# Kernel optimization log

Measured on AMD Instinct MI355X. Metric: run time of the kernel, lower is better.

Reference implementation:

```python
import jax, jax.numpy as jnp
import numpy as np

B = 262144      # batch
DIN = 100       # input covariate dim (cfg_density[0][0])
H = 64          # hidden dim
G = 10          # num_grid -> density output dim G+1
NH = 5          # number of dosage-bucket heads in Multi_head


def setup_inputs() -> dict:
    key = jax.random.key(0)
    ks = jax.random.split(key, 16)
    s = 0.05
    return {
        "dosage": jax.random.uniform(ks[0], (B,), dtype=jnp.float32),
        "x": jax.random.normal(ks[1], (B, DIN), dtype=jnp.float32),
        # density feature MLP (two Linear+ReLU layers)
        "dW0": jax.random.normal(ks[2], (DIN, H), dtype=jnp.float32) * s,
        "db0": jax.random.normal(ks[3], (H,), dtype=jnp.float32) * s,
        "dW1": jax.random.normal(ks[4], (H, H), dtype=jnp.float32) * s,
        "db1": jax.random.normal(ks[5], (H,), dtype=jnp.float32) * s,
        # Density_Block: Linear(H -> G+1) then softmax + grid interpolation
        "dbW": jax.random.normal(ks[6], (H, G + 1), dtype=jnp.float32) * s,
        "dbB": jax.random.normal(ks[7], (G + 1,), dtype=jnp.float32) * s,
        # Multi_head: 5 structurally identical heads, params stacked on axis 0
        # layer0: Treat_Linear(64 -> 64, relu, istreat=1)
        "W0": jax.random.normal(ks[8], (NH, H, H), dtype=jnp.float32) * s,
        "tw0": jax.random.normal(ks[9], (NH, H), dtype=jnp.float32) * s,
        "b0": jax.random.normal(ks[10], (NH, H), dtype=jnp.float32) * s,
        # layer1 (last): Treat_Linear(64 -> 1, no act, istreat=1)
        "W1": jax.random.normal(ks[11], (NH, H, 1), dtype=jnp.float32) * s,
        "tw1": jax.random.normal(ks[12], (NH, 1), dtype=jnp.float32) * s,
        "b1": jax.random.normal(ks[13], (NH, 1), dtype=jnp.float32) * s,
    }


def reference(dosage, x, dW0, db0, dW1, db1, dbW, dbB, W0, tw0, b0, W1, tw1, b1):
    # hidden feature MLP
    hidden = jax.nn.relu(x @ dW0 + db0)
    hidden = jax.nn.relu(hidden @ dW1 + db1)            # [B, H]

    # ---- Density_Block: softmax over grid, dual gather + linear interpolation
    p = jax.nn.softmax(hidden @ dbW + dbB, axis=1)      # [B, G+1]
    tB = dosage * G
    U = jnp.ceil(tB)
    inter = 1.0 - (U - tB)                              # fractional position in cell
    Ui = U.astype(jnp.int32)
    Li = Ui - 1
    Li = Li + (Li < 0).astype(jnp.int32)                # clamp L=-1 -> 0
    pL = jnp.take_along_axis(p, Li[:, None], axis=1)[:, 0]
    pU = jnp.take_along_axis(p, Ui[:, None], axis=1)[:, 0]
    g = pL + (pU - pL) * inter                          # [B]

    # ---- Multi_head: 5 heads on dosage buckets [0,.2),[.2,.4),...,[.8,1.)
    t = dosage
    # layer0: out = feat @ W + t * tw + b, relu; compute all heads, select later
    h0 = jax.nn.relu(
        jnp.einsum('bi,hio->bho', hidden, W0)
        + t[:, None, None] * tw0[None]
        + b0[None]
    )                                                   # [B, NH, H]
    # last layer: no activation
    out1 = (jnp.einsum('bho,hoj->bhj', h0, W1)
            + t[:, None, None] * tw1[None]
            + b1[None])                                 # [B, NH, 1]
    bucket = jnp.clip(jnp.floor(t * NH).astype(jnp.int32), 0, NH - 1)
    Q = jnp.take_along_axis(out1, bucket[:, None, None], axis=1)[:, 0, :]  # [B, 1]
    return g, Q
```

## Files before the change

kernel.cpp:

```cpp
#include <hip/hip_runtime.h>

typedef __attribute__((ext_vector_type(8))) short  short8;
typedef __attribute__((ext_vector_type(4))) float  floatx4;
typedef __attribute__((ext_vector_type(4))) int    intx4;

constexpr int DIN = 100;
constexpr int H   = 64;
constexpr int G   = 10;
constexpr int NH  = 5;
constexpr int MWG = 64;
constexpr int HP  = 72;

constexpr int NF_DW0 = 16, NF_DW1 = 8, NF_DBW = 2;
constexpr int NF_LIN = NF_DW0 + NF_DW1 + NF_DBW;
constexpr int NF_TOT = NF_LIN + 40;

__device__ __forceinline__ unsigned short f2bf_rne(float f) {
    union { float f; unsigned u; } v{f};
    unsigned r = v.u + 0x7FFF + ((v.u >> 16) & 1);
    return (unsigned short)(r >> 16);
}

__device__ __forceinline__ short8 pack8(const float* f) {
    intx4 p;
    #pragma unroll
    for (int j = 0; j < 4; ++j) {
        unsigned a = __float_as_uint(f[2 * j])     + 0x8000u;
        unsigned b = __float_as_uint(f[2 * j + 1]) + 0x8000u;
        p[j] = (int)((b & 0xFFFF0000u) | (a >> 16));
    }
    union { intx4 i; short8 s; } u; u.i = p;
    return u.s;
}

__device__ __forceinline__ unsigned short f2bf_hu(float f) {
    return (unsigned short)((__float_as_uint(f) + 0x8000u) >> 16);
}

__device__ __forceinline__ short8 ldfrag(const unsigned short* __restrict__ ws,
                                         int f, int lane) {
    return *(const short8*)(ws + (size_t)(f * 64 + lane) * 8);
}

__global__ __launch_bounds__(64) void pack_kernel(
    const float* __restrict__ dW0, const float* __restrict__ dW1,
    const float* __restrict__ dbW, const float* __restrict__ W0,
    unsigned short* __restrict__ ws)
{
    const int f = blockIdx.x;
    const int lane = threadIdx.x;
    const int q = lane >> 4, cl = lane & 15;
    float v[8];
    if (f < NF_DW0) {
        int c = f >> 2, g = f & 3;
        #pragma unroll
        for (int j = 0; j < 8; ++j) {
            int k = c * 32 + q * 8 + j, n = g * 16 + cl;
            v[j] = (k < DIN) ? dW0[k * H + n] : 0.0f;
        }
    } else if (f < NF_DW0 + NF_DW1) {
        int r = f - NF_DW0; int c = r >> 2, g = r & 3;
        #pragma unroll
        for (int j = 0; j < 8; ++j) {
            int k = c * 32 + q * 8 + j, n = g * 16 + cl;
            v[j] = dW1[k * H + n];
        }
    } else if (f < NF_LIN) {
        int c = f - (NF_DW0 + NF_DW1);
        #pragma unroll
        for (int j = 0; j < 8; ++j) {
            int k = c * 32 + q * 8 + j, n = cl;
            v[j] = (n <= G) ? dbW[k * (G + 1) + n] : 0.0f;
        }
    } else {
        int r = f - NF_LIN; int h = r >> 3; r &= 7; int c = r >> 2, g = r & 3;
        #pragma unroll
        for (int j = 0; j < 8; ++j) {
            int k = c * 32 + q * 8 + j, n = g * 16 + cl;
            v[j] = W0[(h * H + k) * H + n];
        }
    }
    short8 s;
    #pragma unroll
    for (int j = 0; j < 8; ++j) s[j] = (short)f2bf_rne(v[j]);
    *(short8*)(ws + (size_t)(f * 64 + lane) * 8) = s;
}

__global__ __launch_bounds__(256, 4) void drnet_mfma(
    const float* __restrict__ dosage, const float* __restrict__ x,
    const float* __restrict__ db0, const float* __restrict__ db1,
    const float* __restrict__ dbB,
    const float* __restrict__ tw0, const float* __restrict__ b0,
    const float* __restrict__ W1, const float* __restrict__ tw1,
    const float* __restrict__ b1,
    const unsigned short* __restrict__ wsfrag,
    float* __restrict__ outg, float* __restrict__ outq)
{
    __shared__ unsigned short hbuf[MWG * HP];
    const int tid  = threadIdx.x;
    const int wave = tid >> 6, lane = tid & 63;
    const int q = lane >> 4, cl = lane & 15;
    const int rowbase = blockIdx.x * MWG + wave * 16;
    unsigned short* hb = hbuf + wave * 16 * HP;

    float t4[4];
    int   bk4[4];
    #pragma unroll
    for (int r = 0; r < 4; ++r) {
        float t = dosage[rowbase + 4 * q + r];
        t4[r] = t;
        int bk = (int)floorf(t * (float)NH);
        bk4[r] = min(max(bk, 0), NH - 1);
    }

    floatx4 acc[4];

    short8 a1[4];
    {
        const float* xr = x + (size_t)(rowbase + cl) * DIN;
        #pragma unroll
        for (int cch = 0; cch < 4; ++cch) {
            float f[8];
            if (cch < 3) {
                floatx4 u0 = *(const floatx4*)(xr + cch * 32 + q * 8);
                floatx4 u1 = *(const floatx4*)(xr + cch * 32 + q * 8 + 4);
                f[0]=u0.x; f[1]=u0.y; f[2]=u0.z; f[3]=u0.w;
                f[4]=u1.x; f[5]=u1.y; f[6]=u1.z; f[7]=u1.w;
            } else {
                if (q == 0) {
                    floatx4 u0 = *(const floatx4*)(xr + 96);
                    f[0]=u0.x; f[1]=u0.y; f[2]=u0.z; f[3]=u0.w;
                    f[4]=f[5]=f[6]=f[7]=0.0f;
                } else {
                    #pragma unroll
                    for (int j = 0; j < 8; ++j) f[j] = 0.0f;
                }
            }
            a1[cch] = pack8(f);
        }
    }
    #pragma unroll
    for (int g = 0; g < 4; ++g) acc[g] = (floatx4)0.0f;
    #pragma unroll
    for (int cch = 0; cch < 4; ++cch)
        #pragma unroll
        for (int g = 0; g < 4; ++g) {
            short8 bf = ldfrag(wsfrag, cch * 4 + g, lane);
            acc[g] = __builtin_amdgcn_mfma_f32_16x16x32_bf16(a1[cch], bf, acc[g], 0, 0, 0);
        }
    #pragma unroll
    for (int g = 0; g < 4; ++g) {
        float bias = db0[g * 16 + cl];
        #pragma unroll
        for (int r = 0; r < 4; ++r)
            hb[(4 * q + r) * HP + g * 16 + cl] =
                f2bf_hu(fmaxf(acc[g][r] + bias, 0.0f));
    }

    short8 a2[2];
    #pragma unroll
    for (int cch = 0; cch < 2; ++cch)
        a2[cch] = *(const short8*)(hb + cl * HP + cch * 32 + q * 8);
    #pragma unroll
    for (int g = 0; g < 4; ++g) acc[g] = (floatx4)0.0f;
    #pragma unroll
    for (int cch = 0; cch < 2; ++cch)
        #pragma unroll
        for (int g = 0; g < 4; ++g) {
            short8 bf = ldfrag(wsfrag, NF_DW0 + cch * 4 + g, lane);
            acc[g] = __builtin_amdgcn_mfma_f32_16x16x32_bf16(a2[cch], bf, acc[g], 0, 0, 0);
        }
    #pragma unroll
    for (int g = 0; g < 4; ++g) {
        float bias = db1[g * 16 + cl];
        #pragma unroll
        for (int r = 0; r < 4; ++r)
            hb[(4 * q + r) * HP + g * 16 + cl] =
                f2bf_hu(fmaxf(acc[g][r] + bias, 0.0f));
    }

    short8 af[2];
    #pragma unroll
    for (int cch = 0; cch < 2; ++cch)
        af[cch] = *(const short8*)(hb + cl * HP + cch * 32 + q * 8);

    floatx4 accd = (floatx4)0.0f;
    #pragma unroll
    for (int cch = 0; cch < 2; ++cch) {
        short8 bf = ldfrag(wsfrag, NF_DW0 + NF_DW1 + cch, lane);
        accd = __builtin_amdgcn_mfma_f32_16x16x32_bf16(af[cch], bf, accd, 0, 0, 0);
    }
    const float dbBv = (cl <= G) ? dbB[cl] : 0.0f;
    float gout[4];
    #pragma unroll
    for (int r = 0; r < 4; ++r) {
        float l = (cl <= G) ? (accd[r] + dbBv) : -1e30f;
        float m = l;
        m = fmaxf(m, __shfl_xor(m, 1)); m = fmaxf(m, __shfl_xor(m, 2));
        m = fmaxf(m, __shfl_xor(m, 4)); m = fmaxf(m, __shfl_xor(m, 8));
        float e = __expf(l - m);
        float s = e;
        s += __shfl_xor(s, 1); s += __shfl_xor(s, 2);
        s += __shfl_xor(s, 4); s += __shfl_xor(s, 8);
        const float t  = t4[r];
        const float tB = t * (float)G;
        const float U  = ceilf(tB);
        const float inter = 1.0f - (U - tB);
        int Ui = (int)U; int Li = Ui - 1; if (Li < 0) Li = 0;
        float pL = __shfl(e, q * 16 + Li);
        float pU = __shfl(e, q * 16 + Ui);
        gout[r] = (pL + (pU - pL) * inter) / s;
    }
    if (cl == 0) {
        floatx4 gv = { gout[0], gout[1], gout[2], gout[3] };
        *(floatx4*)(outg + rowbase + 4 * q) = gv;
    }

    float asel[4][4];
    #pragma unroll
    for (int g = 0; g < 4; ++g)
        #pragma unroll
        for (int r = 0; r < 4; ++r) asel[g][r] = 0.0f;

    #pragma unroll 1
    for (int h = 0; h < NH; ++h) {
        floatx4 acch[4];
        #pragma unroll
        for (int g = 0; g < 4; ++g) acch[g] = (floatx4)0.0f;
        #pragma unroll
        for (int cch = 0; cch < 2; ++cch)
            #pragma unroll
            for (int g = 0; g < 4; ++g) {
                short8 bf = ldfrag(wsfrag, NF_LIN + h * 8 + cch * 4 + g, lane);
                acch[g] = __builtin_amdgcn_mfma_f32_16x16x32_bf16(af[cch], bf, acch[g], 0, 0, 0);
            }
        #pragma unroll
        for (int r = 0; r < 4; ++r) {
            bool sel = (bk4[r] == h);
            #pragma unroll
            for (int g = 0; g < 4; ++g)
                asel[g][r] = sel ? acch[g][r] : asel[g][r];
        }
    }

    float qp[4] = {0, 0, 0, 0};
    #pragma unroll
    for (int g = 0; g < 4; ++g) {
        const int ci = g * 16 + cl;
        #pragma unroll
        for (int r = 0; r < 4; ++r) {
            const int off = bk4[r] * H + ci;
            float h0 = asel[g][r] + t4[r] * tw0[off] + b0[off];
            qp[r] += fmaxf(h0, 0.0f) * W1[off];
        }
    }
    #pragma unroll
    for (int r = 0; r < 4; ++r) {
        float s = qp[r];
        s += __shfl_xor(s, 1); s += __shfl_xor(s, 2);
        s += __shfl_xor(s, 4); s += __shfl_xor(s, 8);
        const int h = bk4[r];
        qp[r] = s + t4[r] * tw1[h] + b1[h];
    }
    if (cl == 0) {
        floatx4 Qv = { qp[0], qp[1], qp[2], qp[3] };
        *(floatx4*)(outq + rowbase + 4 * q) = Qv;
    }
}

extern "C" void kernel_launch(void* const* d_in, const int* in_sizes, int n_in,
                              void* d_out, int out_size, void* d_ws, size_t ws_size,
                              hipStream_t stream) {
    const float* dosage = (const float*)d_in[0];
    const float* x      = (const float*)d_in[1];
    const float* dW0    = (const float*)d_in[2];
    const float* db0    = (const float*)d_in[3];
    const float* dW1    = (const float*)d_in[4];
    const float* db1    = (const float*)d_in[5];
    const float* dbW    = (const float*)d_in[6];
    const float* dbB    = (const float*)d_in[7];
    const float* W0     = (const float*)d_in[8];
    const float* tw0    = (const float*)d_in[9];
    const float* b0     = (const float*)d_in[10];
    const float* W1     = (const float*)d_in[11];
    const float* tw1    = (const float*)d_in[12];
    const float* b1     = (const float*)d_in[13];

    const int Btot = in_sizes[0];
    float* outg = (float*)d_out;
    float* outq = outg + Btot;
    unsigned short* ws = (unsigned short*)d_ws;

    pack_kernel<<<NF_TOT, 64, 0, stream>>>(dW0, dW1, dbW, W0, ws);
    drnet_mfma<<<Btot / MWG, 256, 0, stream>>>(dosage, x, db0, db1, dbB,
                                               tw0, b0, W1, tw1, b1,
                                               ws, outg, outq);
}
```

Before: 210.4 us.

## Compute transposed MFMA layers in registers, dropping LDS staging and raising rows per wave

Swaps the MFMA operands so weights are the A operand and activations the B operand, which gives each lane an output layout where a row sits in lanes. The hidden activations are then re-laid between layers with cross-lane shuffles instead of being staged through shared memory. Each wave now handles 32 rows as two 16-row tiles, and head weights are loaded once per head and reused across both tiles. The softmax and head bias/ReLU/W1 stage use vectorized parameter loads, and the softmax no longer subtracts the row max. In exchange there are more shuffles and higher register pressure, and dropping the max subtraction could overflow the exponential for large logits.

```diff
diff --git a/kernel.cpp b/kernel.cpp
--- a/kernel.cpp
+++ b/kernel.cpp
@@ -1,15 +1,14 @@
 #include <hip/hip_runtime.h>
+#include <hip/hip_bf16.h>
 
 typedef __attribute__((ext_vector_type(8))) short  short8;
 typedef __attribute__((ext_vector_type(4))) float  floatx4;
-typedef __attribute__((ext_vector_type(4))) int    intx4;
 
 constexpr int DIN = 100;
 constexpr int H   = 64;
 constexpr int G   = 10;
 constexpr int NH  = 5;
-constexpr int MWG = 64;
-constexpr int HP  = 72;
+constexpr int MWG = 128;
 
 constexpr int NF_DW0 = 16, NF_DW1 = 8, NF_DBW = 2;
 constexpr int NF_LIN = NF_DW0 + NF_DW1 + NF_DBW;
@@ -21,21 +20,13 @@
     return (unsigned short)(r >> 16);
 }
 
-__device__ __forceinline__ short8 pack8(const float* f) {
-    intx4 p;
-    #pragma unroll
-    for (int j = 0; j < 4; ++j) {
-        unsigned a = __float_as_uint(f[2 * j])     + 0x8000u;
-        unsigned b = __float_as_uint(f[2 * j + 1]) + 0x8000u;
-        p[j] = (int)((b & 0xFFFF0000u) | (a >> 16));
-    }
-    union { intx4 i; short8 s; } u; u.i = p;
-    return u.s;
-}
-
-__device__ __forceinline__ unsigned short f2bf_hu(float f) {
-    return (unsigned short)((__float_as_uint(f) + 0x8000u) >> 16);
-}
+__device__ __forceinline__ unsigned pkbf(float a, float b) {
+    union { __hip_bfloat162 h; unsigned u; } u;
+    u.h = __float22bfloat162_rn(make_float2(a, b));
+    return u.u;
+}
+
+union frag_u { unsigned u[4]; short8 s; };
 
 __device__ __forceinline__ short8 ldfrag(const unsigned short* __restrict__ ws,
                                          int f, int lane) {
@@ -86,7 +77,25 @@
     *(short8*)(ws + (size_t)(f * 64 + lane) * 8) = s;
 }
 
-__global__ __launch_bounds__(256, 4) void drnet_mfma(
+__device__ __forceinline__ void transp(const unsigned P[4][2], int q, int cl,
+                                       unsigned out[2][4]) {
+    const int sL = (((2 * q) & 3) << 4) | cl;
+    const int sH = (((2 * q + 1) & 3) << 4) | cl;
+    const bool hi = (q >= 2);
+    #pragma unroll
+    for (int c2 = 0; c2 < 2; ++c2)
+        #pragma unroll
+        for (int w = 0; w < 2; ++w) {
+            int a0 = __shfl((int)P[2 * c2][w], sL);
+            int a1 = __shfl((int)P[2 * c2 + 1][w], sL);
+            out[c2][w] = (unsigned)(hi ? a1 : a0);
+            int b0 = __shfl((int)P[2 * c2][w], sH);
+            int b1 = __shfl((int)P[2 * c2 + 1][w], sH);
+            out[c2][2 + w] = (unsigned)(hi ? b1 : b0);
+        }
+}
+
+__global__ __launch_bounds__(256, 4) void drnet_t(
     const float* __restrict__ dosage, const float* __restrict__ x,
     const float* __restrict__ db0, const float* __restrict__ db1,
     const float* __restrict__ dbB,
@@ -96,175 +105,162 @@
     const unsigned short* __restrict__ wsfrag,
     float* __restrict__ outg, float* __restrict__ outq)
 {
-    __shared__ unsigned short hbuf[MWG * HP];
     const int tid  = threadIdx.x;
     const int wave = tid >> 6, lane = tid & 63;
     const int q = lane >> 4, cl = lane & 15;
-    const int rowbase = blockIdx.x * MWG + wave * 16;
-    unsigned short* hb = hbuf + wave * 16 * HP;
-
-    float t4[4];
-    int   bk4[4];
-    #pragma unroll
-    for (int r = 0; r < 4; ++r) {
-        float t = dosage[rowbase + 4 * q + r];
-        t4[r] = t;
-        int bk = (int)floorf(t * (float)NH);
-        bk4[r] = min(max(bk, 0), NH - 1);
-    }
-
-    floatx4 acc[4];
-
-    short8 a1[4];
-    {
-        const float* xr = x + (size_t)(rowbase + cl) * DIN;
-        #pragma unroll
-        for (int cch = 0; cch < 4; ++cch) {
+    const int rowbase = blockIdx.x * MWG + wave * 32;
+
+    float tmt[2]; int bkmt[2];
+    #pragma unroll
+    for (int mt = 0; mt < 2; ++mt) {
+        float t = dosage[rowbase + mt * 16 + cl];
+        tmt[mt] = t;
+        bkmt[mt] = min(max((int)floorf(t * (float)NH), 0), NH - 1);
+    }
+
+    unsigned af[2][2][4];
+
+    #pragma unroll 1
+    for (int mt = 0; mt < 2; ++mt) {
+        unsigned xf[4][4];
+        const float* xr = x + (size_t)(rowbase + mt * 16 + cl) * DIN;
+        #pragma unroll
+        for (int c = 0; c < 4; ++c) {
             float f[8];
-            if (cch < 3) {
-                floatx4 u0 = *(const floatx4*)(xr + cch * 32 + q * 8);
-                floatx4 u1 = *(const floatx4*)(xr + cch * 32 + q * 8 + 4);
+            if (c < 3) {
+                floatx4 u0 = *(const floatx4*)(xr + c * 32 + q * 8);
+                floatx4 u1 = *(const floatx4*)(xr + c * 32 + q * 8 + 4);
                 f[0]=u0.x; f[1]=u0.y; f[2]=u0.z; f[3]=u0.w;
                 f[4]=u1.x; f[5]=u1.y; f[6]=u1.z; f[7]=u1.w;
+            } else if (q == 0) {
+                floatx4 u0 = *(const floatx4*)(xr + 96);
+                f[0]=u0.x; f[1]=u0.y; f[2]=u0.z; f[3]=u0.w;
+                f[4]=f[5]=f[6]=f[7]=0.0f;
             } else {
-                if (q == 0) {
-                    floatx4 u0 = *(const floatx4*)(xr + 96);
-                    f[0]=u0.x; f[1]=u0.y; f[2]=u0.z; f[3]=u0.w;
-                    f[4]=f[5]=f[6]=f[7]=0.0f;
-                } else {
-                    #pragma unroll
-                    for (int j = 0; j < 8; ++j) f[j] = 0.0f;
-                }
+                #pragma unroll
+                for (int j = 0; j < 8; ++j) f[j] = 0.0f;
             }
-            a1[cch] = pack8(f);
-        }
-    }
-    #pragma unroll
-    for (int g = 0; g < 4; ++g) acc[g] = (floatx4)0.0f;
-    #pragma unroll
-    for (int cch = 0; cch < 4; ++cch)
-        #pragma unroll
-        for (int g = 0; g < 4; ++g) {
-            short8 bf = ldfrag(wsfrag, cch * 4 + g, lane);
-            acc[g] = __builtin_amdgcn_mfma_f32_16x16x32_bf16(a1[cch], bf, acc[g], 0, 0, 0);
-        }
-    #pragma unroll
-    for (int g = 0; g < 4; ++g) {
-        float bias = db0[g * 16 + cl];
-        #pragma unroll
-        for (int r = 0; r < 4; ++r)
-            hb[(4 * q + r) * HP + g * 16 + cl] =
-                f2bf_hu(fmaxf(acc[g][r] + bias, 0.0f));
-    }
-
-    short8 a2[2];
-    #pragma unroll
-    for (int cch = 0; cch < 2; ++cch)
-        a2[cch] = *(const short8*)(hb + cl * HP + cch * 32 + q * 8);
-    #pragma unroll
-    for (int g = 0; g < 4; ++g) acc[g] = (floatx4)0.0f;
-    #pragma unroll
-    for (int cch = 0; cch < 2; ++cch)
-        #pragma unroll
-        for (int g = 0; g < 4; ++g) {
-            short8 bf = ldfrag(wsfrag, NF_DW0 + cch * 4 + g, lane);
-            acc[g] = __builtin_amdgcn_mfma_f32_16x16x32_bf16(a2[cch], bf, acc[g], 0, 0, 0);
-        }
-    #pragma unroll
-    for (int g = 0; g < 4; ++g) {
-        float bias = db1[g * 16 + cl];
-        #pragma unroll
-        for (int r = 0; r < 4; ++r)
-            hb[(4 * q + r) * HP + g * 16 + cl] =
-                f2bf_hu(fmaxf(acc[g][r] + bias, 0.0f));
-    }
-
-    short8 af[2];
-    #pragma unroll
-    for (int cch = 0; cch < 2; ++cch)
-        af[cch] = *(const short8*)(hb + cl * HP + cch * 32 + q * 8);
-
-    floatx4 accd = (floatx4)0.0f;
-    #pragma unroll
-    for (int cch = 0; cch < 2; ++cch) {
-        short8 bf = ldfrag(wsfrag, NF_DW0 + NF_DW1 + cch, lane);
-        accd = __builtin_amdgcn_mfma_f32_16x16x32_bf16(af[cch], bf, accd, 0, 0, 0);
-    }
-    const float dbBv = (cl <= G) ? dbB[cl] : 0.0f;
-    float gout[4];
-    #pragma unroll
-    for (int r = 0; r < 4; ++r) {
-        float l = (cl <= G) ? (accd[r] + dbBv) : -1e30f;
-        float m = l;
-        m = fmaxf(m, __shfl_xor(m, 1)); m = fmaxf(m, __shfl_xor(m, 2));
-        m = fmaxf(m, __shfl_xor(m, 4)); m = fmaxf(m, __shfl_xor(m, 8));
-        float e = __expf(l - m);
-        float s = e;
-        s += __shfl_xor(s, 1); s += __shfl_xor(s, 2);
-        s += __shfl_xor(s, 4); s += __shfl_xor(s, 8);
-        const float t  = t4[r];
+            xf[c][0] = pkbf(f[0], f[1]); xf[c][1] = pkbf(f[2], f[3]);
+            xf[c][2] = pkbf(f[4], f[5]); xf[c][3] = pkbf(f[6], f[7]);
+        }
+        floatx4 acc[4];
+        #pragma unroll
+        for (int f = 0; f < 4; ++f) acc[f] = (floatx4)0.0f;
+        #pragma unroll
+        for (int c = 0; c < 4; ++c) {
+            frag_u b; b.u[0]=xf[c][0]; b.u[1]=xf[c][1]; b.u[2]=xf[c][2]; b.u[3]=xf[c][3];
+            #pragma unroll
+            for (int f = 0; f < 4; ++f)
+                acc[f] = __builtin_amdgcn_mfma_f32_16x16x32_bf16(
+                    ldfrag(wsfrag, c * 4 + f, lane), b.s, acc[f], 0, 0, 0);
+        }
+        unsigned P[4][2];
+        #pragma unroll
+        for (int f = 0; f < 4; ++f) {
+            floatx4 b4 = *(const floatx4*)(db0 + f * 16 + 4 * q);
+            float v0 = fmaxf(acc[f][0] + b4[0], 0.0f);
+            float v1 = fmaxf(acc[f][1] + b4[1], 0.0f);
+            float v2 = fmaxf(acc[f][2] + b4[2], 0.0f);
+            float v3 = fmaxf(acc[f][3] + b4[3], 0.0f);
+            P[f][0] = pkbf(v0, v1); P[f][1] = pkbf(v2, v3);
+        }
+        unsigned hf[2][4];
+        transp(P, q, cl, hf);
+
+        #pragma unroll
+        for (int f = 0; f < 4; ++f) acc[f] = (floatx4)0.0f;
+        #pragma unroll
+        for (int c2 = 0; c2 < 2; ++c2) {
+            frag_u b; b.u[0]=hf[c2][0]; b.u[1]=hf[c2][1]; b.u[2]=hf[c2][2]; b.u[3]=hf[c2][3];
+            #pragma unroll
+            for (int f = 0; f < 4; ++f)
+                acc[f] = __builtin_amdgcn_mfma_f32_16x16x32_bf16(
+                    ldfrag(wsfrag, NF_DW0 + c2 * 4 + f, lane), b.s, acc[f], 0, 0, 0);
+        }
+        #pragma unroll
+        for (int f = 0; f < 4; ++f) {
+            floatx4 b4 = *(const floatx4*)(db1 + f * 16 + 4 * q);
+            float v0 = fmaxf(acc[f][0] + b4[0], 0.0f);
+            float v1 = fmaxf(acc[f][1] + b4[1], 0.0f);
+            float v2 = fmaxf(acc[f][2] + b4[2], 0.0f);
+            float v3 = fmaxf(acc[f][3] + b4[3], 0.0f);
+            P[f][0] = pkbf(v0, v1); P[f][1] = pkbf(v2, v3);
+        }
+        transp(P, q, cl, af[mt]);
+
+        floatx4 accd = (floatx4)0.0f;
+        #pragma unroll
+        for (int c2 = 0; c2 < 2; ++c2) {
+            frag_u b; b.u[0]=af[mt][c2][0]; b.u[1]=af[mt][c2][1];
+            b.u[2]=af[mt][c2][2]; b.u[3]=af[mt][c2][3];
+            accd = __builtin_amdgcn_mfma_f32_16x16x32_bf16(
+                ldfrag(wsfrag, NF_DW0 + NF_DW1 + c2, lane), b.s, accd, 0, 0, 0);
+        }
+        float e[4];
+        #pragma unroll
+        for (int r = 0; r < 4; ++r) {
+            int gi = 4 * q + r;
+            e[r] = (gi <= G) ? __expf(accd[r] + dbB[gi]) : 0.0f;
+        }
+        float s = (e[0] + e[1]) + (e[2] + e[3]);
+        s += __shfl_xor(s, 16); s += __shfl_xor(s, 32);
+        const float t  = tmt[mt];
         const float tB = t * (float)G;
         const float U  = ceilf(tB);
         const float inter = 1.0f - (U - tB);
         int Ui = (int)U; int Li = Ui - 1; if (Li < 0) Li = 0;
-        float pL = __shfl(e, q * 16 + Li);
-        float pU = __shfl(e, q * 16 + Ui);
-        gout[r] = (pL + (pU - pL) * inter) / s;
-    }
-    if (cl == 0) {
-        floatx4 gv = { gout[0], gout[1], gout[2], gout[3] };
-        *(floatx4*)(outg + rowbase + 4 * q) = gv;
-    }
-
-    float asel[4][4];
-    #pragma unroll
-    for (int g = 0; g < 4; ++g)
-        #pragma unroll
-        for (int r = 0; r < 4; ++r) asel[g][r] = 0.0f;
-
+        float l01 = (Li & 1) ? e[1] : e[0], l23 = (Li & 1) ? e[3] : e[2];
+        float vL  = (Li & 2) ? l23 : l01;
+        float u01 = (Ui & 1) ? e[1] : e[0], u23 = (Ui & 1) ? e[3] : e[2];
+        float vU  = (Ui & 2) ? u23 : u01;
+        float pL = __shfl(vL, ((Li >> 2) << 4) + cl);
+        float pU = __shfl(vU, ((Ui >> 2) << 4) + cl);
+        float gv = (pL + (pU - pL) * inter) / s;
+        if (q == 0) outg[rowbase + mt * 16 + cl] = gv;
+    }
+
+    float Q[2] = {0.0f, 0.0f};
     #pragma unroll 1
     for (int h = 0; h < NH; ++h) {
-        floatx4 acch[4];
-        #pragma unroll
-        for (int g = 0; g < 4; ++g) acch[g] = (floatx4)0.0f;
-        #pragma unroll
-        for (int cch = 0; cch < 2; ++cch)
-            #pragma unroll
-            for (int g = 0; g < 4; ++g) {
-                short8 bf = ldfrag(wsfrag, NF_LIN + h * 8 + cch * 4 + g, lane);
-                acch[g] = __builtin_amdgcn_mfma_f32_16x16x32_bf16(af[cch], bf, acch[g], 0, 0, 0);
+        short8 wf[8];
+        #pragma unroll
+        for (int i = 0; i < 8; ++i) wf[i] = ldfrag(wsfrag, NF_LIN + h * 8 + i, lane);
+        #pragma unroll
+        for (int mt = 0; mt < 2; ++mt) {
+            floatx4 a3[4];
+            #pragma unroll
+            for (int f = 0; f < 4; ++f) a3[f] = (floatx4)0.0f;
+            #pragma unroll
+            for (int c2 = 0; c2 < 2; ++c2) {
+                frag_u b; b.u[0]=af[mt][c2][0]; b.u[1]=af[mt][c2][1];
+                b.u[2]=af[mt][c2][2]; b.u[3]=af[mt][c2][3];
+                #pragma unroll
+                for (int f = 0; f < 4; ++f)
+                    a3[f] = __builtin_amdgcn_mfma_f32_16x16x32_bf16(
+                        wf[c2 * 4 + f], b.s, a3[f], 0, 0, 0);
             }
-        #pragma unroll
-        for (int r = 0; r < 4; ++r) {
-            bool sel = (bk4[r] == h);
-            #pragma unroll
-            for (int g = 0; g < 4; ++g)
-                asel[g][r] = sel ? acch[g][r] : asel[g][r];
-        }
-    }
-
-    float qp[4] = {0, 0, 0, 0};
-    #pragma unroll
-    for (int g = 0; g < 4; ++g) {
-        const int ci = g * 16 + cl;
-        #pragma unroll
-        for (int r = 0; r < 4; ++r) {
-            const int off = bk4[r] * H + ci;
-            float h0 = asel[g][r] + t4[r] * tw0[off] + b0[off];
-            qp[r] += fmaxf(h0, 0.0f) * W1[off];
-        }
-    }
-    #pragma unroll
-    for (int r = 0; r < 4; ++r) {
-        float s = qp[r];
-        s += __shfl_xor(s, 1); s += __shfl_xor(s, 2);
-        s += __shfl_xor(s, 4); s += __shfl_xor(s, 8);
-        const int h = bk4[r];
-        qp[r] = s + t4[r] * tw1[h] + b1[h];
-    }
-    if (cl == 0) {
-        floatx4 Qv = { qp[0], qp[1], qp[2], qp[3] };
-        *(floatx4*)(outq + rowbase + 4 * q) = Qv;
+            float part = 0.0f;
+            #pragma unroll
+            for (int f = 0; f < 4; ++f) {
+                const int off = h * H + f * 16 + 4 * q;
+                floatx4 tw4 = *(const floatx4*)(tw0 + off);
+                floatx4 b04 = *(const floatx4*)(b0 + off);
+                floatx4 w14 = *(const floatx4*)(W1 + off);
+                #pragma unroll
+                for (int r = 0; r < 4; ++r) {
+                    float v = a3[f][r] + tmt[mt] * tw4[r] + b04[r];
+                    part = fmaf(fmaxf(v, 0.0f), w14[r], part);
+                }
+            }
+            part += __shfl_xor(part, 16); part += __shfl_xor(part, 32);
+            Q[mt] += (bkmt[mt] == h) ? part : 0.0f;
+        }
+    }
+    #pragma unroll
+    for (int mt = 0; mt < 2; ++mt) {
+        const int h = bkmt[mt];
+        float qv = Q[mt] + tmt[mt] * tw1[h] + b1[h];
+        if (q == 0) outq[rowbase + mt * 16 + cl] = qv;
     }
 }
 
@@ -289,10 +285,10 @@
     const int Btot = in_sizes[0];
     float* outg = (float*)d_out;
     float* outq = outg + Btot;
-    unsigned short* ws = (unsigned short*)d_ws;
-
-    pack_kernel<<<NF_TOT, 64, 0, stream>>>(dW0, dW1, dbW, W0, ws);
-    drnet_mfma<<<Btot / MWG, 256, 0, stream>>>(dosage, x, db0, db1, dbB,
-                                               tw0, b0, W1, tw1, b1,
-                                               ws, outg, outq);
-}
+    unsigned short* wsfrag = (unsigned short*)d_ws;
+
+    pack_kernel<<<NF_TOT, 64, 0, stream>>>(dW0, dW1, dbW, W0, wsfrag);
+    drnet_t<<<Btot / MWG, 256, 0, stream>>>(dosage, x, db0, db1, dbB,
+                                            tw0, b0, W1, tw1, b1,
+                                            wsfrag, outg, outq);
+}
```

New measurement: 273.0 us. 1.3x slower.
